# Performance work log

Measured on AMD Instinct MI355X. Metric: run time of the kernel, lower is better.

The kernel has to match this reference:

```python
import jax, jax.numpy as jnp
import numpy as np

N, K, D, A = 65536, 1024, 256, 64  # batch, n_clusters, s_dim, a_dim
STD_0 = 1.0


@jax.custom_vjp
def grad1abs(x):
    # torch Grad1Abs: forward = |x|, backward flips sign only where x < 0
    # (so grad at exactly 0 is +1, unlike jnp.abs).
    return jnp.abs(x)


def _g1a_fwd(x):
    return jnp.abs(x), x


def _g1a_bwd(x, g):
    return (jnp.where(x < 0, -g, g),)


grad1abs.defvjp(_g1a_fwd, _g1a_bwd)


def setup_inputs() -> dict:
    key = jax.random.key(0)
    k_s, k_c, k_w, k_m = jax.random.split(key, 4)
    return {
        "s": jax.random.normal(k_s, (N, D), dtype=jnp.float32),
        "centers": jax.random.normal(k_c, (K, D), dtype=jnp.float32),
        "c_weights": jax.random.normal(k_w, (K,), dtype=jnp.float32),
        "means": jax.random.normal(k_m, (K, A), dtype=jnp.float32),
        "log_sigma": jnp.full((A,), np.log(STD_0), dtype=jnp.float32),
        "log_temp": jnp.float32(0.0),
    }


def reference(s, centers, c_weights, means, log_sigma, log_temp):
    # squared euclidean distance to centers, computed as a GEMM-friendly
    # expansion of sum((s[:,None,:] - centers[None,:,:])**2, -1): [N, K]
    sq_dist = (
        jnp.sum(s * s, axis=-1, keepdims=True)          # [N, 1]
        + jnp.sum(centers * centers, axis=-1)[None, :]  # [1, K]
        - 2.0 * s @ centers.T                           # [N, K]
    )
    # unnormalized membership: |c_weights| * exp(-exp(log_temp) * dist)
    w = grad1abs(c_weights)[None, :] * jnp.exp(-jnp.exp(log_temp) * sq_dist)
    # normalize with +1 in the denominator (soft "none of the clusters" mass)
    w = w / (jnp.sum(w, axis=-1, keepdims=True) + 1.0)
    mean = w @ means                      # [N, A]
    chol = jnp.diag(jnp.exp(log_sigma))   # [A, A]
    return mean, chol
```

## Files before the change

### kernel.cpp

```cpp
#include <hip/hip_runtime.h>

#define N_ROWS 65536
#define K_CL   1024
#define D_DIM  256
#define A_DIM  64
#define CHUNK  32
#define NCH    (K_CL / CHUNK)
#define CB     8192

#define WS_Q_OFF (K_CL * 256)

typedef float    f32x4 __attribute__((ext_vector_type(4)));
typedef long     l64x2 __attribute__((ext_vector_type(2)));
typedef unsigned u32x4 __attribute__((ext_vector_type(4)));

__device__ __forceinline__ unsigned f2e4m3(float f) {
    unsigned u = __builtin_bit_cast(unsigned, f);
    unsigned sg = (u >> 24) & 0x80u;
    int e8 = (int)((u >> 23) & 0xFF) - 120;
    unsigned m = u & 0x7FFFFFu;
    if (e8 <= 0) return sg;
    unsigned r = m + 0x7FFFFu + ((m >> 20) & 1u);
    m = r >> 20;
    if (m == 8u) { m = 0u; e8 += 1; }
    return sg | ((unsigned)e8 << 3) | m;
}

__global__ __launch_bounds__(256) void prep_kernel(const float* __restrict__ centers,
                                                   const float* __restrict__ cw,
                                                   const float* __restrict__ log_temp,
                                                   unsigned char* __restrict__ ws)
{
    const int tid = threadIdx.x, lane = tid & 63, wid = tid >> 6;
    const float te = __expf(log_temp[0]) * 1.44269504088896340736f;
    #pragma unroll
    for (int i = 0; i < 4; ++i) {
        const int row = blockIdx.x * 16 + wid * 4 + i;
        const f32x4 v = ((const f32x4*)(centers + (long)row * D_DIM))[lane];
        float ss = v.x * v.x + v.y * v.y + v.z * v.z + v.w * v.w;
        #pragma unroll
        for (int m = 1; m < 64; m <<= 1) ss += __shfl_xor(ss, m, 64);
        if (lane == 0)
            ((float*)(ws + WS_Q_OFF))[row] = fmaf(-te, ss, __log2f(fabsf(cw[row])));
    }
    const int tg   = blockIdx.x * 256 + tid;
    const int c    = tg >> 9;
    const int rstp = (tg >> 6) & 7;
    const int l    = tg & 63;
    const int t    = rstp >> 2, ksp = rstp & 3;
    const int lo   = l & 15,    hi  = l >> 4;
    const int col  = c * CHUNK + t * 16 + lo;
    const int k0   = ksp * 64 + hi * 8;
    const float* cp = centers + (long)col * D_DIM;
    const f32x4 a = *(const f32x4*)(cp + k0),      b = *(const f32x4*)(cp + k0 + 4);
    const f32x4 d = *(const f32x4*)(cp + k0 + 32), e = *(const f32x4*)(cp + k0 + 36);
    u32x4 o;
    o.x = f2e4m3(a.x) | (f2e4m3(a.y) << 8) | (f2e4m3(a.z) << 16) | (f2e4m3(a.w) << 24);
    o.y = f2e4m3(b.x) | (f2e4m3(b.y) << 8) | (f2e4m3(b.z) << 16) | (f2e4m3(b.w) << 24);
    o.z = f2e4m3(d.x) | (f2e4m3(d.y) << 8) | (f2e4m3(d.z) << 16) | (f2e4m3(d.w) << 24);
    o.w = f2e4m3(e.x) | (f2e4m3(e.y) << 8) | (f2e4m3(e.z) << 16) | (f2e4m3(e.w) << 24);
    ((u32x4*)ws)[tg] = o;
}

__device__ __attribute__((noinline))
void slow_path(const float* s, const float* centers, const float* cw, const float* means,
               float temp, long brow0, int wid, int lane, float* out)
{
    for (int r2 = 0; r2 < 32; ++r2) {
        const long row = brow0 + wid * 32 + r2;
        const float4 sv = ((const float4*)(s + row * D_DIM))[lane];
        float acc_a = 0.f, rsum = 0.f;
        for (int k = 0; k < K_CL; ++k) {
            const float4 cv = ((const float4*)(centers + (long)k * D_DIM))[lane];
            float d2 = (sv.x - cv.x) * (sv.x - cv.x) + (sv.y - cv.y) * (sv.y - cv.y)
                     + (sv.z - cv.z) * (sv.z - cv.z) + (sv.w - cv.w) * (sv.w - cv.w);
            #pragma unroll
            for (int m = 1; m < 64; m <<= 1) d2 += __shfl_xor(d2, m, 64);
            const float w = fabsf(cw[k]) * __expf(-temp * d2);
            rsum += w;
            acc_a += w * means[k * A_DIM + lane];
        }
        out[row * A_DIM + lane] = acc_a / (rsum + 1.f);
    }
}

__global__ __launch_bounds__(64, 3)
void fused_kernel(const float* __restrict__ s,
                  const unsigned char* __restrict__ ws,
                  const float* __restrict__ means,
                  const float* __restrict__ centers,
                  const float* __restrict__ cw,
                  const float* __restrict__ log_temp,
                  float* __restrict__ out)
{
    const int lane = threadIdx.x & 63;
    const int lo   = lane & 15;
    const int hi   = lane >> 4;
    const long brow0 = (long)blockIdx.x * 32;

    const float temp = __expf(log_temp[0]);
    const float te   = temp * 1.44269504088896340736f;
    const float t2e  = 2.0f * te;

    long afrag[2][8];
    float ssm[2];
    #pragma unroll
    for (int m = 0; m < 2; ++m) {
        const float* srow = s + (brow0 + m * 16 + lo) * D_DIM;
        float ss = 0.f;
        #pragma unroll
        for (int ks = 0; ks < 8; ++ks) {
            const int k0 = ks * 32 + hi * 8;
            const f32x4 u = *(const f32x4*)(srow + k0);
            const f32x4 v = *(const f32x4*)(srow + k0 + 4);
            ss += u.x * u.x + u.y * u.y + u.z * u.z + u.w * u.w;
            ss += v.x * v.x + v.y * v.y + v.z * v.z + v.w * v.w;
            unsigned d0, d1;
#if __has_builtin(__builtin_amdgcn_cvt_pk_fp8_f32)
            d0 = (unsigned)__builtin_amdgcn_cvt_pk_fp8_f32(u.x, u.y, 0, false);
            d0 = (unsigned)__builtin_amdgcn_cvt_pk_fp8_f32(u.z, u.w, (int)d0, true);
            d1 = (unsigned)__builtin_amdgcn_cvt_pk_fp8_f32(v.x, v.y, 0, false);
            d1 = (unsigned)__builtin_amdgcn_cvt_pk_fp8_f32(v.z, v.w, (int)d1, true);
#else
            d0 = f2e4m3(u.x) | (f2e4m3(u.y) << 8) | (f2e4m3(u.z) << 16) | (f2e4m3(u.w) << 24);
            d1 = f2e4m3(v.x) | (f2e4m3(v.y) << 8) | (f2e4m3(v.z) << 16) | (f2e4m3(v.w) << 24);
#endif
            afrag[m][ks] = (long)(((unsigned long long)d1 << 32) | d0);
        }
        ss += __shfl_xor(ss, 16, 64);
        ss += __shfl_xor(ss, 32, 64);
        ssm[m] = ss;
    }
    float a1[2][4];
    #pragma unroll
    for (int m = 0; m < 2; ++m)
        #pragma unroll
        for (int r = 0; r < 4; ++r)
            a1[m][r] = -te * __shfl(ssm[m], hi * 4 + r, 64);

    const float* qptr = (const float*)(ws + WS_Q_OFF);
    float rssum = 0.f;

    l64x2 bbA[8], bbB[8];
    float qA0, qA1, qB0, qB1;

#define LOADB(BB, cc) do {                                                               \
        const unsigned char* _g = ws + (cc) * CB + (lane << 4);                          \
        _Pragma("unroll")                                                                \
        for (int _r = 0; _r < 8; ++_r)                                                   \
            BB[_r] = *(const l64x2*)(_g + _r * 1024);                                    \
    } while (0)

    LOADB(bbA, 0); qA0 = qptr[lo];      qA1 = qptr[16 + lo];
    LOADB(bbB, 1); qB0 = qptr[32 + lo]; qB1 = qptr[48 + lo];

#define STEP(BB, Q0, Q1, cc, PF) do {                                                    \
        f32x4 acc[2][2] = {};                                                            \
        __builtin_amdgcn_s_setprio(1);                                                   \
        _Pragma("unroll")                                                                \
        for (int _ksp = 0; _ksp < 4; ++_ksp) {                                           \
            _Pragma("unroll")                                                            \
            for (int _t = 0; _t < 2; ++_t) {                                             \
                const long _b0 = BB[_t * 4 + _ksp].x;                                    \
                const long _b1 = BB[_t * 4 + _ksp].y;                                    \
                acc[0][_t] = __builtin_amdgcn_mfma_f32_16x16x32_fp8_fp8(afrag[0][2 * _ksp],     _b0, acc[0][_t], 0, 0, 0); \
                acc[1][_t] = __builtin_amdgcn_mfma_f32_16x16x32_fp8_fp8(afrag[1][2 * _ksp],     _b0, acc[1][_t], 0, 0, 0); \
                acc[0][_t] = __builtin_amdgcn_mfma_f32_16x16x32_fp8_fp8(afrag[0][2 * _ksp + 1], _b1, acc[0][_t], 0, 0, 0); \
                acc[1][_t] = __builtin_amdgcn_mfma_f32_16x16x32_fp8_fp8(afrag[1][2 * _ksp + 1], _b1, acc[1][_t], 0, 0, 0); \
            }                                                                            \
        }                                                                                \
        __builtin_amdgcn_s_setprio(0);                                                   \
        const float _cq0 = Q0, _cq1 = Q1;                                                \
        if (PF) {           \
            LOADB(BB, (cc) + 2);                                                         \
            Q0 = qptr[((cc) + 2) * 32 + lo];                                             \
            Q1 = qptr[((cc) + 2) * 32 + 16 + lo];                                        \
        }                                                                                \
        float _arg[2][2][4];                                                             \
        float _amax = -1e30f;                                                            \
        _Pragma("unroll")                                                                \
        for (int _m = 0; _m < 2; ++_m)                                                   \
            _Pragma("unroll")                                                            \
            for (int _r = 0; _r < 4; ++_r) {                                             \
                _arg[_m][0][_r] = fmaf(t2e, acc[_m][0][_r], _cq0 + a1[_m][_r]);          \
                _arg[_m][1][_r] = fmaf(t2e, acc[_m][1][_r], _cq1 + a1[_m][_r]);          \
                _amax = fmaxf(_amax, fmaxf(_arg[_m][0][_r], _arg[_m][1][_r]));           \
            }                                                                            \
              \
        if (__ballot(_amax > -150.0f) != 0ULL) {                                         \
            _Pragma("unroll")                                                            \
            for (int _m = 0; _m < 2; ++_m)                                               \
                _Pragma("unroll")                                                        \
                for (int _t = 0; _t < 2; ++_t)                                           \
                    _Pragma("unroll")                                                    \
                    for (int _r = 0; _r < 4; ++_r) {                                     \
                        float _e;                                                        \
                        asm("v_exp_f32 %0, %1" : "=v"(_e) : "v"(_arg[_m][_t][_r]));      \
                        rssum += _e;                                                     \
                    }                                                                    \
        }                                                                                \
    } while (0)

    #pragma unroll 1
    for (int c2 = 0; c2 < NCH - 4; c2 += 2) {
        STEP(bbA, qA0, qA1, c2, 1);
        STEP(bbB, qB0, qB1, c2 + 1, 1);
    }
    STEP(bbA, qA0, qA1, 28, 1);
    STEP(bbB, qB0, qB1, 29, 1);
    STEP(bbA, qA0, qA1, 30, 0);
    STEP(bbB, qB0, qB1, 31, 0);
#undef STEP
#undef LOADB

    const unsigned long long bal = __ballot(rssum != 0.f);
    if (bal != 0ULL) {
        slow_path(s, centers, cw, means, temp, brow0, 0, lane, out);
    } else {
        const float4 z = {0.f, 0.f, 0.f, 0.f};
        float4* ob = (float4*)(out + brow0 * A_DIM);
        #pragma unroll
        for (int i = 0; i < 8; ++i) ob[lane + 64 * i] = z;
    }
}

__global__ void chol_kernel(const float* __restrict__ log_sigma, float* __restrict__ out2)
{
    const int i = blockIdx.x * 256 + threadIdx.x;
    const int r = i >> 6, c = i & 63;
    out2[i] = (r == c) ? __expf(log_sigma[r]) : 0.0f;
}

extern "C" void kernel_launch(void* const* d_in, const int* in_sizes, int n_in,
                              void* d_out, int out_size, void* d_ws, size_t ws_size,
                              hipStream_t stream)
{
    const float* s       = (const float*)d_in[0];
    const float* centers = (const float*)d_in[1];
    const float* cwts    = (const float*)d_in[2];
    const float* means   = (const float*)d_in[3];
    const float* lsig    = (const float*)d_in[4];
    const float* ltemp   = (const float*)d_in[5];
    float* out = (float*)d_out;
    unsigned char* ws = (unsigned char*)d_ws;

    prep_kernel<<<64, 256, 0, stream>>>(centers, cwts, ltemp, ws);
    fused_kernel<<<N_ROWS / 32, 64, 0, stream>>>(s, ws, means, centers, cwts, ltemp, out);
    chol_kernel<<<(A_DIM * A_DIM) / 256, 256, 0, stream>>>(lsig, out + (long)N_ROWS * A_DIM);
}
```

Before: 45.53 us.

## Switch distance GEMM to 32x32x64 scaled FP8 MFMA with matching fragment layout

```diff
diff --git a/kernel.cpp b/kernel.cpp
--- a/kernel.cpp
+++ b/kernel.cpp
@@ -10,9 +10,12 @@
 
 #define WS_Q_OFF (K_CL * 256)
 
-typedef float    f32x4 __attribute__((ext_vector_type(4)));
-typedef long     l64x2 __attribute__((ext_vector_type(2)));
-typedef unsigned u32x4 __attribute__((ext_vector_type(4)));
+typedef float    f32x4  __attribute__((ext_vector_type(4)));
+typedef float    f32x16 __attribute__((ext_vector_type(16)));
+typedef int      i32x8  __attribute__((ext_vector_type(8)));
+typedef unsigned u32x4  __attribute__((ext_vector_type(4)));
+
+#define UNIT_SCALE 0x7F7F7F7F
 
 __device__ __forceinline__ unsigned f2e4m3(float f) {
     unsigned u = __builtin_bit_cast(unsigned, f);
@@ -24,6 +27,9 @@
     m = r >> 20;
     if (m == 8u) { m = 0u; e8 += 1; }
     return sg | ((unsigned)e8 << 3) | m;
+}
+__device__ __forceinline__ unsigned pack4(f32x4 v) {
+    return f2e4m3(v.x) | (f2e4m3(v.y) << 8) | (f2e4m3(v.z) << 16) | (f2e4m3(v.w) << 24);
 }
 
 __global__ __launch_bounds__(256) void prep_kernel(const float* __restrict__ centers,
@@ -45,21 +51,19 @@
     }
     const int tg   = blockIdx.x * 256 + tid;
     const int c    = tg >> 9;
-    const int rstp = (tg >> 6) & 7;
-    const int l    = tg & 63;
-    const int t    = rstp >> 2, ksp = rstp & 3;
-    const int lo   = l & 15,    hi  = l >> 4;
-    const int col  = c * CHUNK + t * 16 + lo;
-    const int k0   = ksp * 64 + hi * 8;
-    const float* cp = centers + (long)col * D_DIM;
-    const f32x4 a = *(const f32x4*)(cp + k0),      b = *(const f32x4*)(cp + k0 + 4);
-    const f32x4 d = *(const f32x4*)(cp + k0 + 32), e = *(const f32x4*)(cp + k0 + 36);
+    const int rest = tg & 511;
+    const int ksl  = rest >> 7;
+    const int half = (rest >> 6) & 1;
+    const int l    = rest & 63;
+    const int col  = c * CHUNK + (l & 31);
+    const int k0   = ksl * 64 + (l >> 5) * 32 + half * 16;
+    const float* cp = centers + (long)col * D_DIM + k0;
     u32x4 o;
-    o.x = f2e4m3(a.x) | (f2e4m3(a.y) << 8) | (f2e4m3(a.z) << 16) | (f2e4m3(a.w) << 24);
-    o.y = f2e4m3(b.x) | (f2e4m3(b.y) << 8) | (f2e4m3(b.z) << 16) | (f2e4m3(b.w) << 24);
-    o.z = f2e4m3(d.x) | (f2e4m3(d.y) << 8) | (f2e4m3(d.z) << 16) | (f2e4m3(d.w) << 24);
-    o.w = f2e4m3(e.x) | (f2e4m3(e.y) << 8) | (f2e4m3(e.z) << 16) | (f2e4m3(e.w) << 24);
-    ((u32x4*)ws)[tg] = o;
+    o.x = pack4(*(const f32x4*)(cp + 0));
+    o.y = pack4(*(const f32x4*)(cp + 4));
+    o.z = pack4(*(const f32x4*)(cp + 8));
+    o.w = pack4(*(const f32x4*)(cp + 12));
+    *(u32x4*)(ws + (long)c * CB + ksl * 2048 + l * 32 + half * 16) = o;
 }
 
 __device__ __attribute__((noinline))
@@ -84,7 +88,7 @@
     }
 }
 
-__global__ __launch_bounds__(64, 3)
+__global__ __launch_bounds__(64, 2)
 void fused_kernel(const float* __restrict__ s,
                   const unsigned char* __restrict__ ws,
                   const float* __restrict__ means,
@@ -94,122 +98,112 @@
                   float* __restrict__ out)
 {
     const int lane = threadIdx.x & 63;
-    const int lo   = lane & 15;
-    const int hi   = lane >> 4;
+    const int row  = lane & 31;
+    const int h    = lane >> 5;
     const long brow0 = (long)blockIdx.x * 32;
 
     const float temp = __expf(log_temp[0]);
     const float te   = temp * 1.44269504088896340736f;
     const float t2e  = 2.0f * te;
 
-    long afrag[2][8];
-    float ssm[2];
+    i32x8 af[4];
+    float ss = 0.f;
+    {
+        const float* srow = s + (brow0 + row) * D_DIM;
+        #pragma unroll
+        for (int ksl = 0; ksl < 4; ++ksl) {
+            const float* p = srow + ksl * 64 + h * 32;
+            unsigned w[8];
+            #pragma unroll
+            for (int i = 0; i < 4; ++i) {
+                const f32x4 u = *(const f32x4*)(p + i * 8);
+                const f32x4 v = *(const f32x4*)(p + i * 8 + 4);
+                ss += u.x * u.x + u.y * u.y + u.z * u.z + u.w * u.w;
+                ss += v.x * v.x + v.y * v.y + v.z * v.z + v.w * v.w;
+#if __has_builtin(__builtin_amdgcn_cvt_pk_fp8_f32)
+                unsigned d0 = (unsigned)__builtin_amdgcn_cvt_pk_fp8_f32(u.x, u.y, 0, false);
+                d0 = (unsigned)__builtin_amdgcn_cvt_pk_fp8_f32(u.z, u.w, (int)d0, true);
+                unsigned d1 = (unsigned)__builtin_amdgcn_cvt_pk_fp8_f32(v.x, v.y, 0, false);
+                d1 = (unsigned)__builtin_amdgcn_cvt_pk_fp8_f32(v.z, v.w, (int)d1, true);
+#else
+                unsigned d0 = pack4(u), d1 = pack4(v);
+#endif
+                w[2 * i] = d0; w[2 * i + 1] = d1;
+            }
+            af[ksl] = (i32x8){(int)w[0], (int)w[1], (int)w[2], (int)w[3],
+                              (int)w[4], (int)w[5], (int)w[6], (int)w[7]};
+        }
+        ss += __shfl_xor(ss, 32, 64);
+    }
+    float a1[16];
     #pragma unroll
-    for (int m = 0; m < 2; ++m) {
-        const float* srow = s + (brow0 + m * 16 + lo) * D_DIM;
-        float ss = 0.f;
-        #pragma unroll
-        for (int ks = 0; ks < 8; ++ks) {
-            const int k0 = ks * 32 + hi * 8;
-            const f32x4 u = *(const f32x4*)(srow + k0);
-            const f32x4 v = *(const f32x4*)(srow + k0 + 4);
-            ss += u.x * u.x + u.y * u.y + u.z * u.z + u.w * u.w;
-            ss += v.x * v.x + v.y * v.y + v.z * v.z + v.w * v.w;
-            unsigned d0, d1;
-#if __has_builtin(__builtin_amdgcn_cvt_pk_fp8_f32)
-            d0 = (unsigned)__builtin_amdgcn_cvt_pk_fp8_f32(u.x, u.y, 0, false);
-            d0 = (unsigned)__builtin_amdgcn_cvt_pk_fp8_f32(u.z, u.w, (int)d0, true);
-            d1 = (unsigned)__builtin_amdgcn_cvt_pk_fp8_f32(v.x, v.y, 0, false);
-            d1 = (unsigned)__builtin_amdgcn_cvt_pk_fp8_f32(v.z, v.w, (int)d1, true);
-#else
-            d0 = f2e4m3(u.x) | (f2e4m3(u.y) << 8) | (f2e4m3(u.z) << 16) | (f2e4m3(u.w) << 24);
-            d1 = f2e4m3(v.x) | (f2e4m3(v.y) << 8) | (f2e4m3(v.z) << 16) | (f2e4m3(v.w) << 24);
-#endif
-            afrag[m][ks] = (long)(((unsigned long long)d1 << 32) | d0);
-        }
-        ss += __shfl_xor(ss, 16, 64);
-        ss += __shfl_xor(ss, 32, 64);
-        ssm[m] = ss;
-    }
-    float a1[2][4];
-    #pragma unroll
-    for (int m = 0; m < 2; ++m)
-        #pragma unroll
-        for (int r = 0; r < 4; ++r)
-            a1[m][r] = -te * __shfl(ssm[m], hi * 4 + r, 64);
+    for (int r = 0; r < 16; ++r)
+        a1[r] = -te * __shfl(ss, (r & 3) + 8 * (r >> 2) + 4 * h, 64);
 
     const float* qptr = (const float*)(ws + WS_Q_OFF);
     float rssum = 0.f;
 
-    l64x2 bbA[8], bbB[8];
-    float qA0, qA1, qB0, qB1;
+    i32x8 bbA[4], bbB[4];
+    float qA, qB;
 
 #define LOADB(BB, cc) do {                                                               \
-        const unsigned char* _g = ws + (cc) * CB + (lane << 4);                          \
+        const unsigned char* _g = ws + (cc) * CB + (lane << 5);                          \
         _Pragma("unroll")                                                                \
-        for (int _r = 0; _r < 8; ++_r)                                                   \
-            BB[_r] = *(const l64x2*)(_g + _r * 1024);                                    \
+        for (int _r = 0; _r < 4; ++_r)                                                   \
+            BB[_r] = *(const i32x8*)(_g + _r * 2048);                                    \
     } while (0)
 
-    LOADB(bbA, 0); qA0 = qptr[lo];      qA1 = qptr[16 + lo];
-    LOADB(bbB, 1); qB0 = qptr[32 + lo]; qB1 = qptr[48 + lo];
-
-#define STEP(BB, Q0, Q1, cc, PF) do {                                                    \
-        f32x4 acc[2][2] = {};                                                            \
+    LOADB(bbA, 0); qA = qptr[row];
+    LOADB(bbB, 1); qB = qptr[CHUNK + row];
+
+#define STEP(BB, Q, cc, PF) do {                                                         \
+        f32x16 acc = {0.f, 0.f, 0.f, 0.f, 0.f, 0.f, 0.f, 0.f,                            \
+                      0.f, 0.f, 0.f, 0.f, 0.f, 0.f, 0.f, 0.f};                           \
         __builtin_amdgcn_s_setprio(1);                                                   \
-        _Pragma("unroll")                                                                \
-        for (int _ksp = 0; _ksp < 4; ++_ksp) {                                           \
-            _Pragma("unroll")                                                            \
-            for (int _t = 0; _t < 2; ++_t) {                                             \
-                const long _b0 = BB[_t * 4 + _ksp].x;                                    \
-                const long _b1 = BB[_t * 4 + _ksp].y;                                    \
-                acc[0][_t] = __builtin_amdgcn_mfma_f32_16x16x32_fp8_fp8(afrag[0][2 * _ksp],     _b0, acc[0][_t], 0, 0, 0); \
-                acc[1][_t] = __builtin_amdgcn_mfma_f32_16x16x32_fp8_fp8(afrag[1][2 * _ksp],     _b0, acc[1][_t], 0, 0, 0); \
-                acc[0][_t] = __builtin_amdgcn_mfma_f32_16x16x32_fp8_fp8(afrag[0][2 * _ksp + 1], _b1, acc[0][_t], 0, 0, 0); \
-                acc[1][_t] = __builtin_amdgcn_mfma_f32_16x16x32_fp8_fp8(afrag[1][2 * _ksp + 1], _b1, acc[1][_t], 0, 0, 0); \
-            }                                                                            \
-        }                                                                                \
+        acc = __builtin_amdgcn_mfma_scale_f32_32x32x64_f8f6f4(                           \
+                  af[0], BB[0], acc, 0, 0, 0, UNIT_SCALE, 0, UNIT_SCALE);                \
+        acc = __builtin_amdgcn_mfma_scale_f32_32x32x64_f8f6f4(                           \
+                  af[1], BB[1], acc, 0, 0, 0, UNIT_SCALE, 0, UNIT_SCALE);                \
+        acc = __builtin_amdgcn_mfma_scale_f32_32x32x64_f8f6f4(                           \
+                  af[2], BB[2], acc, 0, 0, 0, UNIT_SCALE, 0, UNIT_SCALE);                \
+        acc = __builtin_amdgcn_mfma_scale_f32_32x32x64_f8f6f4(                           \
+                  af[3], BB[3], acc, 0, 0, 0, UNIT_SCALE, 0, UNIT_SCALE);                \
         __builtin_amdgcn_s_setprio(0);                                                   \
-        const float _cq0 = Q0, _cq1 = Q1;                                                \
+        const float _cq = Q;                                                             \
         if (PF) {           \
             LOADB(BB, (cc) + 2);                                                         \
-            Q0 = qptr[((cc) + 2) * 32 + lo];                                             \
-            Q1 = qptr[((cc) + 2) * 32 + 16 + lo];                                        \
+            Q = qptr[((cc) + 2) * CHUNK + row];                                          \
         }                                                                                \
-        float _arg[2][2][4];                                                             \
-        float _amax = -1e30f;                                                            \
+        float _arg[16];                                                                  \
         _Pragma("unroll")                                                                \
-        for (int _m = 0; _m < 2; ++_m)                                                   \
-            _Pragma("unroll")                                                            \
-            for (int _r = 0; _r < 4; ++_r) {                                             \
-                _arg[_m][0][_r] = fmaf(t2e, acc[_m][0][_r], _cq0 + a1[_m][_r]);          \
-                _arg[_m][1][_r] = fmaf(t2e, acc[_m][1][_r], _cq1 + a1[_m][_r]);          \
-                _amax = fmaxf(_amax, fmaxf(_arg[_m][0][_r], _arg[_m][1][_r]));           \
-            }                                                                            \
+        for (int _r = 0; _r < 16; ++_r)                                                  \
+            _arg[_r] = fmaf(t2e, acc[_r], _cq + a1[_r]);                                 \
+        float _mx01 = fmaxf(_arg[0], _arg[1]), _mx23 = fmaxf(_arg[2], _arg[3]);          \
+        float _mx45 = fmaxf(_arg[4], _arg[5]), _mx67 = fmaxf(_arg[6], _arg[7]);          \
+        float _mx89 = fmaxf(_arg[8], _arg[9]), _mxab = fmaxf(_arg[10], _arg[11]);        \
+        float _mxcd = fmaxf(_arg[12], _arg[13]), _mxef = fmaxf(_arg[14], _arg[15]);      \
+        float _amax = fmaxf(fmaxf(fmaxf(_mx01, _mx23), fmaxf(_mx45, _mx67)),             \
+                            fmaxf(fmaxf(_mx89, _mxab), fmaxf(_mxcd, _mxef)));            \
               \
         if (__ballot(_amax > -150.0f) != 0ULL) {                                         \
             _Pragma("unroll")                                                            \
-            for (int _m = 0; _m < 2; ++_m)                                               \
-                _Pragma("unroll")                                                        \
-                for (int _t = 0; _t < 2; ++_t)                                           \
-                    _Pragma("unroll")                                                    \
-                    for (int _r = 0; _r < 4; ++_r) {                                     \
-                        float _e;                                                        \
-                        asm("v_exp_f32 %0, %1" : "=v"(_e) : "v"(_arg[_m][_t][_r]));      \
-                        rssum += _e;                                                     \
-                    }                                                                    \
+            for (int _r = 0; _r < 16; ++_r) {                                            \
+                float _e;                                                                \
+                asm("v_exp_f32 %0, %1" : "=v"(_e) : "v"(_arg[_r]));                      \
+                rssum += _e;                                                             \
+            }                                                                            \
         }                                                                                \
     } while (0)
 
     #pragma unroll 1
     for (int c2 = 0; c2 < NCH - 4; c2 += 2) {
-        STEP(bbA, qA0, qA1, c2, 1);
-        STEP(bbB, qB0, qB1, c2 + 1, 1);
-    }
-    STEP(bbA, qA0, qA1, 28, 1);
-    STEP(bbB, qB0, qB1, 29, 1);
-    STEP(bbA, qA0, qA1, 30, 0);
-    STEP(bbB, qB0, qB1, 31, 0);
+        STEP(bbA, qA, c2, 1);
+        STEP(bbB, qB, c2 + 1, 1);
+    }
+    STEP(bbA, qA, 28, 1);
+    STEP(bbB, qB, 29, 1);
+    STEP(bbA, qA, 30, 0);
+    STEP(bbB, qB, 31, 0);
 #undef STEP
 #undef LOADB
 
```

Result: faster. 44.60 us (-2.0%).
